# Performance work log

Hardware: AMD Instinct MI355X
Metric: run time of the kernel (lower is better)

The kernel has to match this reference:

```python
import jax, jax.numpy as jnp
import numpy as np

NODE_LEN = 200000; E = 1000000; BATCH = 128; NT = 2048
IN_FEATS = 256; HID = 128; L1 = 13; L2 = 30; NHEAD = 8; GAMMA = 0.1


def _type_att(xs, W, b, q):
    # xs: [N, T, d] -> [N, d]; type-level (semantic) attention
    s = jnp.einsum('ntd,d->nt', jnp.tanh(xs @ W + b), q)
    a = jax.nn.softmax(s, axis=1)
    return jnp.einsum('nt,ntd->nd', a, xs)


def _add_att(qv, kv, Wq, Wk, v):
    # qv: [N, d], kv: [N, L, d] -> [N, d]; additive attention over L
    t = jnp.tanh((qv @ Wq)[:, None, :] + kv @ Wk)
    a = jax.nn.softmax(jnp.einsum('nld,d->nl', t, v), axis=1)
    return jnp.einsum('nl,nld->nd', a, kv)


def _mha(h, W, b):
    # h: [N, L, D]; W: [4, D, D] (q,k,v,o); b: [4, D]
    N, L, D = h.shape
    hd = D // NHEAD
    def proj(i):
        return (h @ W[i] + b[i]).reshape(N, L, NHEAD, hd).transpose(0, 2, 1, 3)
    q, k, v = proj(0), proj(1), proj(2)
    a = jax.nn.softmax(jnp.einsum('nhld,nhmd->nhlm', q, k) / jnp.sqrt(jnp.float32(hd)), axis=-1)
    o = jnp.einsum('nhlm,nhmd->nhld', a, v).transpose(0, 2, 1, 3).reshape(N, L, D)
    return o @ W[3] + b[3]


def _forward(x, edge_index, batch, rootindex, type_x0, type_x1, type_x2, root1, parent1,
             root2, parent2, type_x3, root3, type_x4, root4, adj,
             W1, b1, W2, b2, mha_W, mha_b, att_Wq, att_Wk, att_v, fuse_W, fuse_b,
             gat_W, gat_a_src, gat_a_dst, ta_W, ta_b, ta_q, gc2_W, gc2_b, fin_W, fin_b):
    n = x.shape[0]
    loop = jnp.arange(n, dtype=edge_index.dtype)
    row = jnp.concatenate([edge_index[0], loop])
    col = jnp.concatenate([edge_index[1], loop])
    deg = jax.ops.segment_sum(jnp.ones(row.shape[0], x.dtype), col, num_segments=n)
    dinv = jax.lax.rsqrt(jnp.maximum(deg, 1.0))
    norm = (dinv[row] * dinv[col])[:, None]

    def gcn(h, W, b):
        m = (h @ W)[row] * norm
        return jax.ops.segment_sum(m, col, num_segments=n) + b

    h1 = gcn(x, W1, b1)                          # conv1
    root_extend = h1[rootindex[batch]]           # per-graph root broadcast (replaces python loop)
    h = jax.nn.relu(jnp.concatenate([h1, root_extend], axis=1))
    h2 = jax.nn.relu(gcn(h, W2, b2))             # conv2
    # sentinel zero row == eye(node_len+1, node_len) one-hot gather semantics
    hp = jnp.concatenate([h2, jnp.zeros((1, h2.shape[1]), h2.dtype)], axis=0)

    x0 = [hp[type_x0]]
    for i, (tx, rid, pid) in enumerate([(type_x1, root1, parent1), (type_x2, root2, parent2)]):
        lst, rt, pr = hp[tx], hp[rid], hp[pid]
        ids = jnp.stack([pr, rt], axis=1)        # [N, 2, d]
        att = _add_att(lst, ids, att_Wq[i], att_Wk[i], att_v[i])
        alpha = jax.nn.sigmoid(jnp.concatenate([lst, att], axis=-1) @ fuse_W[i] + fuse_b[i])[:, None]
        x0.append(alpha * lst + (1.0 - alpha) * att)
    for i, (tx, rid) in enumerate([(type_x3, root3), (type_x4, root4)]):
        seq = _mha(hp[tx], mha_W[i], mha_b[i])   # [N, L, d]
        rt = hp[rid]
        att = _add_att(rt, seq, att_Wq[2 + i], att_Wk[2 + i], att_v[2 + i])
        alpha = jax.nn.sigmoid(jnp.concatenate([rt, att], axis=-1) @ fuse_W[2 + i] + fuse_b[2 + i])[:, None]
        x0.append(alpha * rt + (1.0 - alpha) * att)
    x0.append(hp[type_x0])

    # heterogeneous graph attention conv (gc1) + per-type attention fusion (at1)
    H = jnp.stack([x0[t] @ gat_W[t] for t in range(6)])  # [6, NT, d]
    mask = adj > 0
    x1 = []
    for t1 in range(6):
        msgs = []
        for t2 in range(6):
            e = (H[t1] @ gat_a_src[t1, t2])[:, None] + (H[t2] @ gat_a_dst[t1, t2])[None, :]
            s = jnp.where(mask[t1, t2], jax.nn.leaky_relu(e, negative_slope=GAMMA), -1e9)
            msgs.append(jax.nn.softmax(s, axis=1) @ H[t2])
        m = jnp.stack(msgs, axis=1)                      # [NT, 6, d]
        x1.append(jax.nn.relu(_type_att(m, ta_W[t1], ta_b[t1], ta_q[t1])))
    X1 = jnp.stack(x1)                                   # [6, NT, d]

    # second hop: dense GraphConvolution (gc2) + at2; only type 5 feeds the head
    hx = X1 @ gc2_W
    msgs5 = jnp.einsum('snm,smd->snd', adj[5], hx) + gc2_b
    x2_5 = _type_att(msgs5.transpose(1, 0, 2), ta_W[11], ta_b[11], ta_q[11])
    return jax.nn.log_softmax(x2_5 @ fin_W + fin_b, axis=-1)


def setup_inputs() -> dict:
    key = jax.random.key(0)
    ks = jax.random.split(key, 32)
    f32 = jnp.float32
    x = jax.random.normal(ks[0], (NODE_LEN, IN_FEATS), f32)
    edge_index = jax.random.randint(ks[1], (2, E), 0, NODE_LEN, dtype=jnp.int32)
    batch = jax.random.randint(ks[2], (NODE_LEN,), 0, BATCH, dtype=jnp.int32)
    rootindex = jax.random.randint(ks[3], (BATCH,), 0, NODE_LEN, dtype=jnp.int32)
    idx = lambda k, shape: jax.random.randint(k, shape, 0, NODE_LEN, dtype=jnp.int32)
    type_x0 = idx(ks[4], (NT,)); type_x1 = idx(ks[5], (NT,)); type_x2 = idx(ks[6], (NT,))
    root1 = idx(ks[7], (NT,)); parent1 = idx(ks[8], (NT,))
    root2 = idx(ks[9], (NT,)); parent2 = idx(ks[10], (NT,))
    type_x3 = idx(ks[11], (NT, L1)); root3 = idx(ks[12], (NT,))
    type_x4 = idx(ks[13], (NT, L2)); root4 = idx(ks[14], (NT,))
    adj = (jax.random.uniform(ks[15], (6, 6, NT, NT)) < 0.02).astype(f32)
    p = lambda k, shape: 0.02 * jax.random.normal(k, shape, f32)
    W1 = p(ks[16], (IN_FEATS, HID)); b1 = jnp.zeros((HID,), f32)
    W2 = p(ks[17], (2 * HID, HID)); b2 = jnp.zeros((HID,), f32)
    mha_W = p(ks[18], (2, 4, HID, HID)); mha_b = jnp.zeros((2, 4, HID), f32)
    att_Wq = p(ks[19], (4, HID, HID)); att_Wk = p(ks[20], (4, HID, HID)); att_v = p(ks[21], (4, HID))
    fuse_W = p(ks[22], (4, 2 * HID)); fuse_b = jnp.zeros((4,), f32)
    gat_W = p(ks[23], (6, HID, HID)); gat_a_src = p(ks[24], (6, 6, HID)); gat_a_dst = p(ks[25], (6, 6, HID))
    ta_W = p(ks[26], (12, HID, HID)); ta_b = jnp.zeros((12, HID), f32); ta_q = p(ks[27], (12, HID))
    gc2_W = p(ks[28], (HID, HID)); gc2_b = jnp.zeros((HID,), f32)
    fin_W = p(ks[29], (HID, 4)); fin_b = jnp.zeros((4,), f32)
    return dict(x=x, edge_index=edge_index, batch=batch, rootindex=rootindex,
                type_x0=type_x0, type_x1=type_x1, type_x2=type_x2,
                root1=root1, parent1=parent1, root2=root2, parent2=parent2,
                type_x3=type_x3, root3=root3, type_x4=type_x4, root4=root4, adj=adj,
                W1=W1, b1=b1, W2=W2, b2=b2, mha_W=mha_W, mha_b=mha_b,
                att_Wq=att_Wq, att_Wk=att_Wk, att_v=att_v, fuse_W=fuse_W, fuse_b=fuse_b,
                gat_W=gat_W, gat_a_src=gat_a_src, gat_a_dst=gat_a_dst,
                ta_W=ta_W, ta_b=ta_b, ta_q=ta_q, gc2_W=gc2_W, gc2_b=gc2_b,
                fin_W=fin_W, fin_b=fin_b)


def reference(x, edge_index, batch, rootindex, type_x0, type_x1, type_x2, root1, parent1,
              root2, parent2, type_x3, root3, type_x4, root4, adj,
              W1, b1, W2, b2, mha_W, mha_b, att_Wq, att_Wk, att_v, fuse_W, fuse_b,
              gat_W, gat_a_src, gat_a_dst, ta_W, ta_b, ta_q, gc2_W, gc2_b, fin_W, fin_b):
    return _forward(x, edge_index, batch, rootindex, type_x0, type_x1, type_x2, root1, parent1,
                    root2, parent2, type_x3, root3, type_x4, root4, adj,
                    W1, b1, W2, b2, mha_W, mha_b, att_Wq, att_Wk, att_v, fuse_W, fuse_b,
                    gat_W, gat_a_src, gat_a_dst, ta_W, ta_b, ta_q, gc2_W, gc2_b, fin_W, fin_b)
```

## Files before the change

### kernel.cpp

```cpp
#include <hip/hip_runtime.h>
#include <hip/hip_bf16.h>
#include <math.h>


typedef unsigned short u16;
typedef unsigned int   u32;
typedef __attribute__((ext_vector_type(8))) short short8;
typedef __attribute__((ext_vector_type(4))) float f32x4;

#define NNODE 200000
#define NEDGE 1000000
#define NTT   2048

static constexpr size_t MiB = 1024ull * 1024ull;

enum : unsigned {
    O_W1 = 0,         O_b1 = 32768,     O_W2 = 32896,     O_b2 = 65664,
    O_mhaW = 65792,   O_mhab = 196864,  O_attWq = 197888, O_attWk = 263424,
    O_attv = 328960,  O_fuseW = 329472, O_fuseb = 330496, O_gatW = 330504,
    O_asrc = 428808,  O_adst = 433416,  O_taW = 438024,   O_tab = 634632,
    O_taq = 636168,   O_gc2W = 637704,  O_gc2b = 654088,  O_finW = 654216,
    O_finb = 654728
};
enum : unsigned {
    T_W1 = 0,          T_W2 = 32768,     T_mhaW = 65536,   T_attWk = 196608,
    T_gatW = 262144,   T_taW = 360448,   T_gc2W = 557056
};

__device__ __forceinline__ float b2f(u16 u) { return __uint_as_float(((u32)u) << 16); }
__device__ __forceinline__ u16 f2b(float f) {
    u32 u = __float_as_uint(f);
    u32 r = (u + 0x7fffu + ((u >> 16) & 1u)) >> 16;
    return (u16)r;
}

__device__ __forceinline__ float wsum(float v) {
#pragma unroll
    for (int m = 1; m < 64; m <<= 1) v += __shfl_xor(v, m, 64);
    return v;
}
__device__ __forceinline__ float bsum128(float v, float* s) {
    v = wsum(v);
    __syncthreads();
    if ((threadIdx.x & 63) == 0) s[threadIdx.x >> 6] = v;
    __syncthreads();
    return s[0] + s[1];
}
__device__ __forceinline__ float bmax128(float v, float* s) {
#pragma unroll
    for (int m = 1; m < 64; m <<= 1) v = fmaxf(v, __shfl_xor(v, m, 64));
    __syncthreads();
    if ((threadIdx.x & 63) == 0) s[threadIdx.x >> 6] = v;
    __syncthreads();
    return fmaxf(s[0], s[1]);
}

__global__ __launch_bounds__(256) void probe_k(const void* xsrc, int* flag) {
    __shared__ int cnt;
    if (threadIdx.x == 0) cnt = 0;
    __syncthreads();
    int c = 0;
    for (int i = threadIdx.x; i < 4096; i += 256) {
        float v = fabsf(b2f(((const u16*)xsrc)[2 * i]));
        if (v > 1e-6f && v < 100.f) c++;
    }
    atomicAdd(&cnt, c);
    __syncthreads();
    if (threadIdx.x == 0) {
        flag[0] = (cnt < 2048) ? 1 : 0;
        flag[1] = 1;
    }
}

struct CEnt { const void* src; unsigned dstOff; unsigned cnt; };
struct CTab { CEnt e[21]; };
struct TEnt { const void* src; unsigned dstOff; unsigned cnt; int msh; int ksh; };
struct TTab { TEnt e[7]; };
__global__ __launch_bounds__(256) void convp_k(CTab tb, TTab tt, u16* pb, u16* pbT,
                                               const int* flag) {
    bool f32 = flag[0] != 0;
    int stride = gridDim.x * blockDim.x;
    int tid = blockIdx.x * blockDim.x + threadIdx.x;
    for (int k = 0; k < 21; k++) {
        const void* s = tb.e[k].src;
        unsigned off = tb.e[k].dstOff, n = tb.e[k].cnt;
        for (unsigned i = tid; i < n; i += stride)
            pb[off + i] = f32 ? f2b(((const float*)s)[i]) : ((const u16*)s)[i];
    }
    for (int k = 0; k < 7; k++) {
        const void* s = tt.e[k].src;
        unsigned off = tt.e[k].dstOff, n = tt.e[k].cnt;
        int msh = tt.e[k].msh, ksh = tt.e[k].ksh;
        for (unsigned i = tid; i < n; i += stride) {
            unsigned mat = i >> msh, r = i & ((1u << msh) - 1);
            unsigned kk = r >> 7, nn = r & 127;
            unsigned dst = (mat << msh) + (nn << ksh) + kk;
            pbT[off + dst] = f32 ? f2b(((const float*)s)[i]) : ((const u16*)s)[i];
        }
    }
}

template <int K, bool OBF>
__global__ __launch_bounds__(256) void gemm_bf16(const void* __restrict__ A,
                                                 const u16* __restrict__ WT,
                                                 const u16* __restrict__ bias,
                                                 void* __restrict__ Cv, int M,
                                                 const int* flagp) {
    constexpr int LW = 40;
    __shared__ u16 Al[128 * LW];
    __shared__ u16 Bl[128 * LW];
    const int tid = threadIdx.x;
    const int lane = tid & 63, wv = tid >> 6;
    const int row0 = blockIdx.x * 128;
    const int m16 = lane & 15, oct = lane >> 4;
    const bool aF32 = flagp && (flagp[0] != 0);

    f32x4 acc[2][8];
#pragma unroll
    for (int s = 0; s < 2; s++)
#pragma unroll
        for (int t = 0; t < 8; t++) acc[s][t] = (f32x4){0.f, 0.f, 0.f, 0.f};

    const int r = tid >> 1, kk16 = (tid & 1) * 16;
    const int gr = row0 + r;
    const bool rowOk = (gr < M);

    for (int k0 = 0; k0 < K; k0 += 32) {
        {
            uint4 d0 = {0, 0, 0, 0}, d1 = {0, 0, 0, 0};
            if (rowOk) {
                if (aF32) {
                    const float4* s4 = (const float4*)((const float*)A + (size_t)gr * K + k0 + kk16);
                    union { uint4 v[2]; u16 u[16]; } t;
#pragma unroll
                    for (int q = 0; q < 4; q++) {
                        float4 f = s4[q];
                        t.u[q * 4 + 0] = f2b(f.x); t.u[q * 4 + 1] = f2b(f.y);
                        t.u[q * 4 + 2] = f2b(f.z); t.u[q * 4 + 3] = f2b(f.w);
                    }
                    d0 = t.v[0];
                    d1 = t.v[1];
                } else {
                    const uint4* src = (const uint4*)((const u16*)A + (size_t)gr * K + k0 + kk16);
                    d0 = src[0];
                    d1 = src[1];
                }
            }
            *(uint4*)&Al[r * LW + kk16] = d0;
            *(uint4*)&Al[r * LW + kk16 + 8] = d1;
        }
        {
            const uint4* wsrc = (const uint4*)(WT + (size_t)r * K + k0 + kk16);
            *(uint4*)&Bl[r * LW + kk16] = wsrc[0];
            *(uint4*)&Bl[r * LW + kk16 + 8] = wsrc[1];
        }
        __syncthreads();

        short8 af0 = *(const short8*)&Al[(wv * 32 + m16) * LW + oct * 8];
        short8 af1 = *(const short8*)&Al[(wv * 32 + 16 + m16) * LW + oct * 8];
        short8 bf[8];
#pragma unroll
        for (int t = 0; t < 8; t++)
            bf[t] = *(const short8*)&Bl[(t * 16 + m16) * LW + oct * 8];
#pragma unroll
        for (int t = 0; t < 8; t++) {
            acc[0][t] = __builtin_amdgcn_mfma_f32_16x16x32_bf16(af0, bf[t], acc[0][t], 0, 0, 0);
            acc[1][t] = __builtin_amdgcn_mfma_f32_16x16x32_bf16(af1, bf[t], acc[1][t], 0, 0, 0);
        }
        __syncthreads();
    }

    float bv[8];
#pragma unroll
    for (int t = 0; t < 8; t++) bv[t] = bias ? b2f(bias[t * 16 + m16]) : 0.f;
#pragma unroll
    for (int s = 0; s < 2; s++)
#pragma unroll
        for (int t = 0; t < 8; t++)
#pragma unroll
            for (int rr = 0; rr < 4; rr++) {
                int orow = row0 + wv * 32 + s * 16 + oct * 4 + rr;
                if (orow < M) {
                    float val = acc[s][t][rr] + bv[t];
                    size_t idx = (size_t)orow * 128 + t * 16 + m16;
                    if (OBF) ((u16*)Cv)[idx] = f2b(val);
                    else     ((float*)Cv)[idx] = val;
                }
            }
}

template <int K, bool OBF>
__global__ __launch_bounds__(256) void gemm_bat_k(const u16* __restrict__ A0, size_t Astride,
                                                  const u16* __restrict__ W0, unsigned Wstride,
                                                  const u16* __restrict__ bias0, unsigned bStride,
                                                  void* __restrict__ Cv, size_t Cstride,
                                                  int M) {
    constexpr int LW = 40;
    __shared__ u16 Al[128 * LW];
    __shared__ u16 Bl[128 * LW];
    const int y = blockIdx.y;
    const u16* A = A0 + (size_t)y * Astride;
    const u16* WT = W0 + (size_t)y * Wstride;
    const u16* bias = bias0 ? (bias0 + (size_t)y * bStride) : nullptr;
    const size_t cbase = (size_t)y * Cstride;
    const int tid = threadIdx.x;
    const int lane = tid & 63, wv = tid >> 6;
    const int row0 = blockIdx.x * 128;
    const int m16 = lane & 15, oct = lane >> 4;

    f32x4 acc[2][8];
#pragma unroll
    for (int s = 0; s < 2; s++)
#pragma unroll
        for (int t = 0; t < 8; t++) acc[s][t] = (f32x4){0.f, 0.f, 0.f, 0.f};

    const int r = tid >> 1, kk16 = (tid & 1) * 16;
    const int gr = row0 + r;
    const bool rowOk = (gr < M);

    for (int k0 = 0; k0 < K; k0 += 32) {
        {
            uint4 d0 = {0, 0, 0, 0}, d1 = {0, 0, 0, 0};
            if (rowOk) {
                const uint4* src = (const uint4*)(A + (size_t)gr * K + k0 + kk16);
                d0 = src[0];
                d1 = src[1];
            }
            *(uint4*)&Al[r * LW + kk16] = d0;
            *(uint4*)&Al[r * LW + kk16 + 8] = d1;
        }
        {
            const uint4* wsrc = (const uint4*)(WT + (size_t)r * K + k0 + kk16);
            *(uint4*)&Bl[r * LW + kk16] = wsrc[0];
            *(uint4*)&Bl[r * LW + kk16 + 8] = wsrc[1];
        }
        __syncthreads();

        short8 af0 = *(const short8*)&Al[(wv * 32 + m16) * LW + oct * 8];
        short8 af1 = *(const short8*)&Al[(wv * 32 + 16 + m16) * LW + oct * 8];
        short8 bf[8];
#pragma unroll
        for (int t = 0; t < 8; t++)
            bf[t] = *(const short8*)&Bl[(t * 16 + m16) * LW + oct * 8];
#pragma unroll
        for (int t = 0; t < 8; t++) {
            acc[0][t] = __builtin_amdgcn_mfma_f32_16x16x32_bf16(af0, bf[t], acc[0][t], 0, 0, 0);
            acc[1][t] = __builtin_amdgcn_mfma_f32_16x16x32_bf16(af1, bf[t], acc[1][t], 0, 0, 0);
        }
        __syncthreads();
    }

    float bv[8];
#pragma unroll
    for (int t = 0; t < 8; t++) bv[t] = bias ? b2f(bias[t * 16 + m16]) : 0.f;
#pragma unroll
    for (int s = 0; s < 2; s++)
#pragma unroll
        for (int t = 0; t < 8; t++)
#pragma unroll
            for (int rr = 0; rr < 4; rr++) {
                int orow = row0 + wv * 32 + s * 16 + oct * 4 + rr;
                if (orow < M) {
                    float val = acc[s][t][rr] + bv[t];
                    size_t idx = cbase + (size_t)orow * 128 + t * 16 + m16;
                    if (OBF) ((u16*)Cv)[idx] = f2b(val);
                    else     ((float*)Cv)[idx] = val;
                }
            }
}

__global__ __launch_bounds__(256) void gemm_conv2(const u16* __restrict__ h1r,
                                                  const int* __restrict__ batch,
                                                  const int* __restrict__ rootindex,
                                                  const u16* __restrict__ WT,
                                                  u16* __restrict__ C, int M) {
    constexpr int LW = 40;
    __shared__ u16 Al[128 * LW];
    __shared__ u16 Bl[128 * LW];
    const int tid = threadIdx.x;
    const int lane = tid & 63, wv = tid >> 6;
    const int row0 = blockIdx.x * 128;
    const int m16 = lane & 15, oct = lane >> 4;

    f32x4 acc[2][8];
#pragma unroll
    for (int s = 0; s < 2; s++)
#pragma unroll
        for (int t = 0; t < 8; t++) acc[s][t] = (f32x4){0.f, 0.f, 0.f, 0.f};

    const int r = tid >> 1, kk16 = (tid & 1) * 16;
    const int gr = row0 + r;
    const u16* pSelf = nullptr; const u16* pRoot = nullptr;
    if (gr < M) {
        pSelf = h1r + (size_t)gr * 128;
        pRoot = h1r + (size_t)rootindex[batch[gr]] * 128;
    }

    for (int k0 = 0; k0 < 256; k0 += 32) {
        {
            int kg = k0 + kk16;
            uint4 d0 = {0, 0, 0, 0}, d1 = {0, 0, 0, 0};
            if (pSelf) {
                const u16* sp = (kg < 128) ? (pSelf + kg) : (pRoot + kg - 128);
                d0 = ((const uint4*)sp)[0];
                d1 = ((const uint4*)sp)[1];
            }
            *(uint4*)&Al[r * LW + kk16] = d0;
            *(uint4*)&Al[r * LW + kk16 + 8] = d1;
        }
        {
            const uint4* wsrc = (const uint4*)(WT + (size_t)r * 256 + k0 + kk16);
            *(uint4*)&Bl[r * LW + kk16] = wsrc[0];
            *(uint4*)&Bl[r * LW + kk16 + 8] = wsrc[1];
        }
        __syncthreads();

        short8 af0 = *(const short8*)&Al[(wv * 32 + m16) * LW + oct * 8];
        short8 af1 = *(const short8*)&Al[(wv * 32 + 16 + m16) * LW + oct * 8];
        short8 bf[8];
#pragma unroll
        for (int t = 0; t < 8; t++)
            bf[t] = *(const short8*)&Bl[(t * 16 + m16) * LW + oct * 8];
#pragma unroll
        for (int t = 0; t < 8; t++) {
            acc[0][t] = __builtin_amdgcn_mfma_f32_16x16x32_bf16(af0, bf[t], acc[0][t], 0, 0, 0);
            acc[1][t] = __builtin_amdgcn_mfma_f32_16x16x32_bf16(af1, bf[t], acc[1][t], 0, 0, 0);
        }
        __syncthreads();
    }
#pragma unroll
    for (int s = 0; s < 2; s++)
#pragma unroll
        for (int t = 0; t < 8; t++)
#pragma unroll
            for (int rr = 0; rr < 4; rr++) {
                int orow = row0 + wv * 32 + s * 16 + oct * 4 + rr;
                if (orow < M)
                    C[(size_t)orow * 128 + t * 16 + m16] = f2b(acc[s][t][rr]);
            }
}

__global__ __launch_bounds__(256) void hist_k(const int* __restrict__ ei,
                                              int* __restrict__ cnt) {
    int e = blockIdx.x * 256 + threadIdx.x;
    if (e < NEDGE) atomicAdd(&cnt[ei[NEDGE + e]], 1);
}
__global__ __launch_bounds__(256) void scan1_k(const int* __restrict__ cnt,
                                               int* __restrict__ bsum) {
    int t = threadIdx.x;
    int base = blockIdx.x * 1024 + t * 4;
    int s = 0;
#pragma unroll
    for (int q = 0; q < 4; q++) {
        int i = base + q;
        if (i < NNODE) s += cnt[i];
    }
#pragma unroll
    for (int m = 1; m < 64; m <<= 1) s += __shfl_xor(s, m, 64);
    __shared__ int ws_[4];
    if ((t & 63) == 0) ws_[t >> 6] = s;
    __syncthreads();
    if (t == 0) bsum[blockIdx.x] = ws_[0] + ws_[1] + ws_[2] + ws_[3];
}
__global__ __launch_bounds__(64) void scan2_k(const int* __restrict__ bsum,
                                              int* __restrict__ bofs, int nb,
                                              int* __restrict__ rowptrN) {
    if (threadIdx.x == 0) {
        int r = 0;
        for (int i = 0; i < nb; i++) { int v = bsum[i]; bofs[i] = r; r += v; }
        *rowptrN = r;
    }
}
__global__ __launch_bounds__(256) void scan3_k(const int* __restrict__ cnt,
                                               const int* __restrict__ bofs,
                                               int* __restrict__ rowptr,
                                               int* __restrict__ cursor,
                                               float* __restrict__ dinv) {
    int t = threadIdx.x, lane = t & 63, wv = t >> 6;
    int base = blockIdx.x * 1024 + t * 4;
    int v[4];
    int s = 0;
#pragma unroll
    for (int q = 0; q < 4; q++) {
        int i = base + q;
        v[q] = (i < NNODE) ? cnt[i] : 0;
        s += v[q];
    }
    int inc = s;
#pragma unroll
    for (int d = 1; d < 64; d <<= 1) {
        int u = __shfl_up(inc, d, 64);
        if (lane >= d) inc += u;
    }
    __shared__ int wsum_[4];
    if (lane == 63) wsum_[wv] = inc;
    __syncthreads();
    int wofs = 0;
    for (int w = 0; w < wv; w++) wofs += wsum_[w];
    int ex = bofs[blockIdx.x] + wofs + inc - s;
#pragma unroll
    for (int q = 0; q < 4; q++) {
        int i = base + q;
        if (i < NNODE) {
            rowptr[i] = ex;
            cursor[i] = ex;
            dinv[i] = rsqrtf((float)(v[q] + 1));
        }
        ex += v[q];
    }
}
__global__ __launch_bounds__(256) void fill_k(const int* __restrict__ ei,
                                              int* __restrict__ cursor,
                                              int* __restrict__ csr_src) {
    int e = blockIdx.x * 256 + threadIdx.x;
    if (e < NEDGE) {
        int col = ei[NEDGE + e];
        int pos = atomicAdd(&cursor[col], 1);
        csr_src[pos] = ei[e];
    }
}
template <bool OBF>
__global__ __launch_bounds__(256) void gather_gcn_k(const u16* __restrict__ xwb,
                                                    const int* __restrict__ rowptr,
                                                    const int* __restrict__ csr_src,
                                                    const float* __restrict__ dinv,
                                                    const u16* __restrict__ bias,
                                                    void* __restrict__ out) {
    int node = blockIdx.x * 4 + (threadIdx.x >> 6);
    if (node >= NNODE) return;
    int lane = threadIdx.x & 63;
    int beg = rowptr[node], end = rowptr[node + 1];
    int cnt = end - beg;
    if (cnt < 0) cnt = 0;
    if (cnt > 2048) cnt = 2048;
    end = beg + cnt;
    float di = dinv[node];
    u32 pk = *(const u32*)&xwb[(size_t)node * 128 + lane * 2];
    float selfn = di * di;
    float a0 = b2f((u16)(pk & 0xffffu)) * selfn;
    float a1 = b2f((u16)(pk >> 16)) * selfn;
    int myrow = 0; float mynrm = 0.f;
    if (lane < cnt) {
        myrow = csr_src[beg + lane];
        mynrm = dinv[myrow] * di;
    }
    int n0 = cnt < 64 ? cnt : 64;
    for (int j = 0; j < n0; j++) {
        int row = __shfl(myrow, j, 64);
        float nrm = __shfl(mynrm, j, 64);
        u32 p2 = *(const u32*)&xwb[(size_t)row * 128 + lane * 2];
        a0 += b2f((u16)(p2 & 0xffffu)) * nrm;
        a1 += b2f((u16)(p2 >> 16)) * nrm;
    }
    for (int j = beg + 64; j < end; j++) {
        int row = csr_src[j];
        float nrm = dinv[row] * di;
        u32 p2 = *(const u32*)&xwb[(size_t)row * 128 + lane * 2];
        a0 += b2f((u16)(p2 & 0xffffu)) * nrm;
        a1 += b2f((u16)(p2 >> 16)) * nrm;
    }
    a0 = fmaxf(a0 + b2f(bias[lane * 2]), 0.f);
    a1 = fmaxf(a1 + b2f(bias[lane * 2 + 1]), 0.f);
    if (OBF) {
        u32 w = (u32)f2b(a0) | ((u32)f2b(a1) << 16);
        *(u32*)&((u16*)out)[(size_t)node * 128 + lane * 2] = w;
    } else {
        float* op = (float*)out + (size_t)node * 128 + lane * 2;
        op[0] = a0;
        op[1] = a1;
    }
}

__global__ __launch_bounds__(256) void x0copy_k(const float* h2, const int* tx, u16* x0) {
    int idx = blockIdx.x * 256 + threadIdx.x;
    int n = idx >> 7, c = idx & 127;
    u16 v = f2b(h2[(size_t)tx[n] * 128 + c]);
    x0[idx] = v;
    x0[5 * NTT * 128 + idx] = v;
}
__global__ __launch_bounds__(256) void gather_seq_k(const float* h2, const int* tx,
                                                    u16* seqb, int total) {
    int idx = blockIdx.x * 256 + threadIdx.x;
    if (idx >= total) return;
    int node = tx[idx >> 7];
    seqb[idx] = f2b(h2[(size_t)node * 128 + (idx & 127)]);
}
__global__ __launch_bounds__(128) void addatt12_k(const float* __restrict__ h2,
                                                  const int* tx, const int* rid, const int* pid,
                                                  const u16* __restrict__ Wq,
                                                  const u16* __restrict__ Wk,
                                                  const u16* __restrict__ vv,
                                                  const u16* __restrict__ fw,
                                                  const u16* fbp, int fbi,
                                                  u16* __restrict__ out) {
    int n = blockIdx.x, c = threadIdx.x;
    __shared__ float ls[128], pr[128], rt[128], red[2];
    ls[c] = h2[(size_t)tx[n] * 128 + c];
    pr[c] = h2[(size_t)pid[n] * 128 + c];
    rt[c] = h2[(size_t)rid[n] * 128 + c];
    __syncthreads();
    float qc = 0.f;
    for (int k = 0; k < 128; k++) qc += ls[k] * b2f(Wq[k * 128 + c]);
    float vc = b2f(vv[c]);
    float u0 = qc, u1 = qc;
    for (int k = 0; k < 128; k++) {
        float wk = b2f(Wk[k * 128 + c]);
        u0 += pr[k] * wk;
        u1 += rt[k] * wk;
    }
    float s0 = bsum128(tanhf(u0) * vc, red);
    float s1 = bsum128(tanhf(u1) * vc, red);
    float mx = fmaxf(s0, s1);
    float e0 = expf(s0 - mx), e1 = expf(s1 - mx);
    float iz = 1.f / (e0 + e1);
    float att = (e0 * pr[c] + e1 * rt[c]) * iz;
    float pa = ls[c] * b2f(fw[c]) + att * b2f(fw[128 + c]);
    float alpha = 1.f / (1.f + expf(-(bsum128(pa, red) + b2f(fbp[fbi]))));
    out[(size_t)n * 128 + c] = f2b(alpha * ls[c] + (1.f - alpha) * att);
}
__global__ __launch_bounds__(64) void mha_attn_k(const u16* __restrict__ q,
                                                 const u16* __restrict__ k,
                                                 const u16* __restrict__ v,
                                                 u16* __restrict__ ao, int L) {
    int n = blockIdx.x, h = blockIdx.y, t = threadIdx.x;
    __shared__ float qs[30][16], ks[30][16], vs[30][16], sc[30][30];
    for (int e = t; e < L * 16; e += 64) {
        int l = e >> 4, d = e & 15;
        size_t base = ((size_t)n * L + l) * 128 + h * 16 + d;
        qs[l][d] = b2f(q[base]);
        ks[l][d] = b2f(k[base]);
        vs[l][d] = b2f(v[base]);
    }
    __syncthreads();
    for (int e = t; e < L * L; e += 64) {
        int l = e / L, m = e % L;
        float s = 0.f;
#pragma unroll
        for (int d = 0; d < 16; d++) s += qs[l][d] * ks[m][d];
        sc[l][m] = s * 0.25f;
    }
    __syncthreads();
    if (t < L) {
        float mx = -3e38f;
        for (int m = 0; m < L; m++) mx = fmaxf(mx, sc[t][m]);
        float z = 0.f;
        for (int m = 0; m < L; m++) { float w = expf(sc[t][m] - mx); sc[t][m] = w; z += w; }
        float izz = 1.f / z;
        for (int m = 0; m < L; m++) sc[t][m] *= izz;
    }
    __syncthreads();
    for (int e = t; e < L * 16; e += 64) {
        int l = e >> 4, d = e & 15;
        float o = 0.f;
        for (int m = 0; m < L; m++) o += sc[l][m] * vs[m][d];
        ao[((size_t)n * L + l) * 128 + h * 16 + d] = f2b(o);
    }
}
__global__ __launch_bounds__(128) void addatt_root_k(const u16* __restrict__ seqo,
                                                     const u16* __restrict__ kpre,
                                                     const float* __restrict__ h2,
                                                     const int* rid,
                                                     const u16* __restrict__ Wq,
                                                     const u16* __restrict__ vv,
                                                     const u16* __restrict__ fw,
                                                     const u16* fbp, int fbi, int L,
                                                     u16* __restrict__ out) {
    int n = blockIdx.x, c = threadIdx.x;
    __shared__ float rt[128], sl[32], red[2];
    rt[c] = h2[(size_t)rid[n] * 128 + c];
    __syncthreads();
    float qc = 0.f;
    for (int k = 0; k < 128; k++) qc += rt[k] * b2f(Wq[k * 128 + c]);
    float vc = b2f(vv[c]);
    for (int l = 0; l < L; l++) {
        float u = qc + b2f(kpre[((size_t)n * L + l) * 128 + c]);
        float s = bsum128(tanhf(u) * vc, red);
        if (c == 0) sl[l] = s;
    }
    __syncthreads();
    float mx = -3e38f;
    for (int l = 0; l < L; l++) mx = fmaxf(mx, sl[l]);
    float z = 0.f;
    for (int l = 0; l < L; l++) z += expf(sl[l] - mx);
    float att = 0.f;
    for (int l = 0; l < L; l++)
        att += expf(sl[l] - mx) * b2f(seqo[((size_t)n * L + l) * 128 + c]);
    att /= z;
    float pa = rt[c] * b2f(fw[c]) + att * b2f(fw[128 + c]);
    float alpha = 1.f / (1.f + expf(-(bsum128(pa, red) + b2f(fbp[fbi]))));
    out[(size_t)n * 128 + c] = f2b(alpha * rt[c] + (1.f - alpha) * att);
}
__global__ __launch_bounds__(128) void gat_e2_k(const float* __restrict__ H,
                                                const u16* __restrict__ asrc,
                                                const u16* __restrict__ adst,
                                                float* esrc, float* edst) {
    int p = blockIdx.y, t1 = p / 6, t2 = p % 6;
    int t = threadIdx.x;
    __shared__ float vs[128], vd[128];
    vs[t] = b2f(asrc[p * 128 + t]);
    vd[t] = b2f(adst[p * 128 + t]);
    __syncthreads();
    int row = t >> 2, part = t & 3;
    int i = blockIdx.x * 32 + row;
    const float4* r1 = (const float4*)(H + ((size_t)t1 * NTT + i) * 128 + part * 32);
    const float4* r2 = (const float4*)(H + ((size_t)t2 * NTT + i) * 128 + part * 32);
    float s1 = 0.f, s2 = 0.f;
#pragma unroll
    for (int q = 0; q < 8; q++) {
        float4 a = r1[q], b = r2[q];
        int kb = part * 32 + q * 4;
        s1 += a.x * vs[kb] + a.y * vs[kb + 1] + a.z * vs[kb + 2] + a.w * vs[kb + 3];
        s2 += b.x * vd[kb] + b.y * vd[kb + 1] + b.z * vd[kb + 2] + b.w * vd[kb + 3];
    }
    s1 += __shfl_xor(s1, 1, 64); s1 += __shfl_xor(s1, 2, 64);
    s2 += __shfl_xor(s2, 1, 64); s2 += __shfl_xor(s2, 2, 64);
    if (part == 0) {
        esrc[p * NTT + i] = s1;
        edst[p * NTT + i] = s2;
    }
}
__global__ __launch_bounds__(128) void gc1_attn_k(const void* __restrict__ adjv,
                                                  const float* __restrict__ H,
                                                  const float* __restrict__ esrc,
                                                  const float* __restrict__ edst,
                                                  u16* __restrict__ msgs,
                                                  const int* flagp) {
    int i = blockIdx.x, p = blockIdx.y, t = threadIdx.x;
    int t2 = p % 6;
    const bool f32 = flagp[0] != 0;
    size_t rowoff = ((size_t)p * NTT + i) * NTT;
    const float* edp = edst + p * NTT;
    float es = esrc[p * NTT + i];
    __shared__ int nzj[2048];
    __shared__ float nzs[2048];
    __shared__ int cnt;
    __shared__ float red[2];
    if (t == 0) cnt = 0;
    __syncthreads();
    int j0 = t * 16;
    float av[16];
    if (f32) {
        const float4* af = (const float4*)((const float*)adjv + rowoff + j0);
#pragma unroll
        for (int q = 0; q < 4; q++) {
            float4 d = af[q];
            av[q * 4 + 0] = d.x; av[q * 4 + 1] = d.y;
            av[q * 4 + 2] = d.z; av[q * 4 + 3] = d.w;
        }
    } else {
        const u16* ab = (const u16*)adjv + rowoff + j0;
        union { uint4 v; u16 u[8]; } a0, a1;
        a0.v = *(const uint4*)(ab);
        a1.v = *(const uint4*)(ab + 8);
#pragma unroll
        for (int q = 0; q < 16; q++) av[q] = b2f(q < 8 ? a0.u[q] : a1.u[q - 8]);
    }
    float lmax = -3e38f;
#pragma unroll
    for (int jj = 0; jj < 16; jj++) {
        if (av[jj] > 0.f) {
            int j = j0 + jj;
            float e = es + edp[j];
            float sv = e > 0.f ? e : 0.1f * e;
            lmax = fmaxf(lmax, sv);
            int kk = atomicAdd(&cnt, 1);
            nzj[kk] = j;
            nzs[kk] = sv;
        }
    }
    float mx = bmax128(lmax, red);
    int nnz = cnt;
    float psum = 0.f;
    for (int k = t; k < nnz; k += 128) {
        float w = expf(nzs[k] - mx);
        nzs[k] = w;
        psum += w;
    }
    float Z = bsum128(psum, red);
    const float* Ht = H + (size_t)t2 * NTT * 128;
    float acc = 0.f;
    if (nnz > 0) {
        for (int k = 0; k < nnz; k++) acc += nzs[k] * Ht[(size_t)nzj[k] * 128 + t];
        acc /= Z;
    } else {
        for (int j = 0; j < NTT; j++) acc += Ht[(size_t)j * 128 + t];
        acc *= (1.f / 2048.f);
    }
    msgs[((size_t)p * NTT + i) * 128 + t] = f2b(acc);
}
__global__ __launch_bounds__(128) void at1_lite_k(const u16* __restrict__ msgs,
                                                  const u16* __restrict__ ubuf,
                                                  const u16* __restrict__ taq,
                                                  u16* __restrict__ X1) {
    int n = blockIdx.x, t1 = blockIdx.y, c = threadIdx.x;
    __shared__ float sv[6], red[2];
    float qcv = b2f(taq[t1 * 128 + c]);
    for (int t2 = 0; t2 < 6; t2++) {
        float u = b2f(ubuf[(((size_t)t1 * 6 + t2) * NTT + n) * 128 + c]);
        float s = bsum128(tanhf(u) * qcv, red);
        if (c == 0) sv[t2] = s;
    }
    __syncthreads();
    float mx = -3e38f;
    for (int t2 = 0; t2 < 6; t2++) mx = fmaxf(mx, sv[t2]);
    float z = 0.f;
    for (int t2 = 0; t2 < 6; t2++) z += expf(sv[t2] - mx);
    float o = 0.f;
    for (int t2 = 0; t2 < 6; t2++)
        o += expf(sv[t2] - mx) * b2f(msgs[(((size_t)t1 * 6 + t2) * NTT + n) * 128 + c]);
    o /= z;
    X1[((size_t)t1 * NTT + n) * 128 + c] = f2b(fmaxf(o, 0.f));
}
__global__ __launch_bounds__(128) void gc2_agg_k(const void* __restrict__ adjv,
                                                 size_t adjBase,
                                                 const float* __restrict__ hx,
                                                 const u16* __restrict__ bias,
                                                 float* __restrict__ msgs5,
                                                 const int* flagp) {
    int i = blockIdx.x, s = blockIdx.y, t = threadIdx.x;
    const bool f32 = flagp[0] != 0;
    size_t rowoff = adjBase + ((size_t)s * NTT + i) * NTT;
    __shared__ int nzj[2048];
    __shared__ float nzw[2048];
    __shared__ int cnt;
    if (t == 0) cnt = 0;
    __syncthreads();
    int j0 = t * 16;
    float av[16];
    if (f32) {
        const float4* af = (const float4*)((const float*)adjv + rowoff + j0);
#pragma unroll
        for (int q = 0; q < 4; q++) {
            float4 d = af[q];
            av[q * 4 + 0] = d.x; av[q * 4 + 1] = d.y;
            av[q * 4 + 2] = d.z; av[q * 4 + 3] = d.w;
        }
    } else {
        const u16* ab = (const u16*)adjv + rowoff + j0;
        union { uint4 v; u16 u[8]; } a0, a1;
        a0.v = *(const uint4*)(ab);
        a1.v = *(const uint4*)(ab + 8);
#pragma unroll
        for (int q = 0; q < 16; q++) av[q] = b2f(q < 8 ? a0.u[q] : a1.u[q - 8]);
    }
#pragma unroll
    for (int jj = 0; jj < 16; jj++) {
        if (av[jj] != 0.f) {
            int kk = atomicAdd(&cnt, 1);
            nzj[kk] = j0 + jj;
            nzw[kk] = av[jj];
        }
    }
    __syncthreads();
    const float* hxs = hx + (size_t)s * NTT * 128;
    float acc = 0.f;
    int nnz = cnt;
    for (int k = 0; k < nnz; k++) acc += nzw[k] * hxs[(size_t)nzj[k] * 128 + t];
    msgs5[((size_t)s * NTT + i) * 128 + t] = acc + b2f(bias[t]);
}
__global__ __launch_bounds__(128) void at2_head_lite_k(const float* __restrict__ msgs5,
                                                       const u16* __restrict__ ubuf2,
                                                       const u16* __restrict__ taq,
                                                       const u16* __restrict__ finW,
                                                       const u16* __restrict__ finb,
                                                       float* __restrict__ out) {
    int n = blockIdx.x, c = threadIdx.x;
    __shared__ float sv[6], red[2];
    float qcv = b2f(taq[11 * 128 + c]);
    for (int s = 0; s < 6; s++) {
        float u = b2f(ubuf2[((size_t)s * NTT + n) * 128 + c]);
        float sc = bsum128(tanhf(u) * qcv, red);
        if (c == 0) sv[s] = sc;
    }
    __syncthreads();
    float mx = -3e38f;
    for (int s = 0; s < 6; s++) mx = fmaxf(mx, sv[s]);
    float z = 0.f;
    for (int s = 0; s < 6; s++) z += expf(sv[s] - mx);
    float x2c = 0.f;
    for (int s = 0; s < 6; s++)
        x2c += expf(sv[s] - mx) * msgs5[((size_t)s * NTT + n) * 128 + c];
    x2c /= z;
    float l0 = bsum128(x2c * b2f(finW[c * 4 + 0]), red) + b2f(finb[0]);
    float l1 = bsum128(x2c * b2f(finW[c * 4 + 1]), red) + b2f(finb[1]);
    float l2 = bsum128(x2c * b2f(finW[c * 4 + 2]), red) + b2f(finb[2]);
    float l3 = bsum128(x2c * b2f(finW[c * 4 + 3]), red) + b2f(finb[3]);
    float m4 = fmaxf(fmaxf(l0, l1), fmaxf(l2, l3));
    float ls = logf(expf(l0 - m4) + expf(l1 - m4) + expf(l2 - m4) + expf(l3 - m4)) + m4;
    if (c < 4) {
        float v = (c == 0) ? l0 : (c == 1) ? l1 : (c == 2) ? l2 : l3;
        out[n * 4 + c] = v - ls;
    }
}

extern "C" void kernel_launch(void* const* d_in, const int* in_sizes, int n_in,
                              void* d_out, int out_size, void* d_ws, size_t ws_size,
                              hipStream_t stream) {
    const void* x       = d_in[0];
    const int* ei       = (const int*)d_in[1];
    const int* batch    = (const int*)d_in[2];
    const int* rootidx  = (const int*)d_in[3];
    const int* type_x0  = (const int*)d_in[4];
    const int* type_x1  = (const int*)d_in[5];
    const int* type_x2  = (const int*)d_in[6];
    const int* root1    = (const int*)d_in[7];
    const int* parent1  = (const int*)d_in[8];
    const int* root2    = (const int*)d_in[9];
    const int* parent2  = (const int*)d_in[10];
    const int* type_x3  = (const int*)d_in[11];
    const int* root3    = (const int*)d_in[12];
    const int* type_x4  = (const int*)d_in[13];
    const int* root4    = (const int*)d_in[14];
    const void* adj     = d_in[15];

    char* ws = (char*)d_ws;
    int*   flag = (int*)(ws);
    u16*   pb   = (u16*)  (ws + 64 * 1024);
    float* dinv = (float*)(ws + 2 * MiB);
    u16*   xwb  = (u16*)  (ws + 3 * MiB);
    float* h2   = (float*)(ws + 52 * MiB);
    u16*   h1r  = (u16*)  (ws + 52 * MiB);
    int*   cnt_i   = (int*)(ws + 150 * MiB);
    int*   rowptr  = (int*)(ws + 151 * MiB);
    int*   cursor  = (int*)(ws + 152 * MiB);
    int*   csr_src = (int*)(ws + 153 * MiB);
    int*   bsum    = (int*)(ws + 158 * MiB);
    int*   bofs    = (int*)(ws + 158 * MiB + 4096);
    u16*   seqb = (u16*)  (ws + 3 * MiB);
    u16*   qb   = (u16*)  (ws + 18 * MiB);
    u16*   kb   = (u16*)  (ws + 33 * MiB);
    u16*   vb   = (u16*)  (ws + 150 * MiB);
    u16*   aob  = (u16*)  (ws + 165 * MiB);
    u16*   seqo = (u16*)  (ws + 18 * MiB);
    u16*   kpre = (u16*)  (ws + 33 * MiB);
    u16*   x0b  = (u16*)  (ws + 180 * MiB);
    u16*   X1b  = (u16*)  (ws + 183 * MiB);
    float* Hb   = (float*)(ws + 52 * MiB);
    float* esrc = (float*)(ws + 58 * MiB);
    float* edst = (float*)(ws + 59 * MiB);
    u16*   msgs = (u16*)  (ws + 60 * MiB);
    u16*   ubuf = (u16*)  (ws + 78 * MiB);
    float* hx   = (float*)(ws + 96 * MiB);
    float* msg5 = (float*)(ws + 102 * MiB);
    u16*   ubuf2= (u16*)  (ws + 60 * MiB);
    u16*   pbT  = (u16*)  (ws + 186 * MiB);

    probe_k<<<1, 256, 0, stream>>>(x, flag);
    CTab tb;
    int kk = 0;
    auto add = [&](int i, unsigned off, unsigned n) {
        tb.e[kk].src = d_in[i]; tb.e[kk].dstOff = off; tb.e[kk].cnt = n; kk++;
    };
    add(16, O_W1, 32768);   add(17, O_b1, 128);     add(18, O_W2, 32768);
    add(19, O_b2, 128);     add(20, O_mhaW, 131072);add(21, O_mhab, 1024);
    add(22, O_attWq, 65536);add(23, O_attWk, 65536);add(24, O_attv, 512);
    add(25, O_fuseW, 1024); add(26, O_fuseb, 4);    add(27, O_gatW, 98304);
    add(28, O_asrc, 4608);  add(29, O_adst, 4608);  add(30, O_taW, 196608);
    add(31, O_tab, 1536);   add(32, O_taq, 1536);   add(33, O_gc2W, 16384);
    add(34, O_gc2b, 128);   add(35, O_finW, 512);   add(36, O_finb, 4);
    TTab tt;
    int tk = 0;
    auto addt = [&](int i, unsigned off, unsigned n, int msh, int ksh) {
        tt.e[tk].src = d_in[i]; tt.e[tk].dstOff = off; tt.e[tk].cnt = n;
        tt.e[tk].msh = msh; tt.e[tk].ksh = ksh; tk++;
    };
    addt(16, T_W1, 32768, 15, 8);
    addt(18, T_W2, 32768, 15, 8);
    addt(20, T_mhaW, 131072, 14, 7);
    addt(23, T_attWk, 65536, 14, 7);
    addt(27, T_gatW, 98304, 14, 7);
    addt(30, T_taW, 196608, 14, 7);
    addt(33, T_gc2W, 16384, 14, 7);
    convp_k<<<256, 256, 0, stream>>>(tb, tt, pb, pbT, flag);

    const int NB = (NNODE + 1023) / 1024;
    hipMemsetAsync(cnt_i, 0, (size_t)NNODE * 4, stream);
    hist_k<<<(NEDGE + 255) / 256, 256, 0, stream>>>(ei, cnt_i);
    scan1_k<<<NB, 256, 0, stream>>>(cnt_i, bsum);
    scan2_k<<<1, 64, 0, stream>>>(bsum, bofs, NB, rowptr + NNODE);
    scan3_k<<<NB, 256, 0, stream>>>(cnt_i, bofs, rowptr, cursor, dinv);
    fill_k<<<(NEDGE + 255) / 256, 256, 0, stream>>>(ei, cursor, csr_src);

    gemm_bf16<256, true><<<(NNODE + 127) / 128, 256, 0, stream>>>(x, pbT + T_W1, (const u16*)nullptr, xwb, NNODE, flag);
    gather_gcn_k<true><<<(NNODE + 3) / 4, 256, 0, stream>>>(xwb, rowptr, csr_src, dinv, pb + O_b1, h1r);

    gemm_conv2<<<(NNODE + 127) / 128, 256, 0, stream>>>(h1r, batch, rootidx, pbT + T_W2, xwb, NNODE);
    gather_gcn_k<false><<<(NNODE + 3) / 4, 256, 0, stream>>>(xwb, rowptr, csr_src, dinv, pb + O_b2, h2);

    x0copy_k<<<(NTT * 128) / 256, 256, 0, stream>>>(h2, type_x0, x0b);
    addatt12_k<<<NTT, 128, 0, stream>>>(h2, type_x1, root1, parent1,
                                        pb + O_attWq, pb + O_attWk, pb + O_attv,
                                        pb + O_fuseW, pb + O_fuseb, 0,
                                        x0b + 1 * NTT * 128);
    addatt12_k<<<NTT, 128, 0, stream>>>(h2, type_x2, root2, parent2,
                                        pb + O_attWq + 16384, pb + O_attWk + 16384,
                                        pb + O_attv + 128, pb + O_fuseW + 256,
                                        pb + O_fuseb, 1,
                                        x0b + 2 * NTT * 128);
    for (int i = 0; i < 2; i++) {
        int L = i ? 30 : 13;
        const int* tx = i ? type_x4 : type_x3;
        const int* rt = i ? root4 : root3;
        int M = NTT * L;
        gather_seq_k<<<(M * 128 + 255) / 256, 256, 0, stream>>>(h2, tx, seqb, M * 128);
        gemm_bf16<128, true><<<(M + 127) / 128, 256, 0, stream>>>(seqb, pbT + T_mhaW + (i * 4 + 0) * 16384,
                                                                  pb + O_mhab + (i * 4 + 0) * 128, qb, M, nullptr);
        gemm_bf16<128, true><<<(M + 127) / 128, 256, 0, stream>>>(seqb, pbT + T_mhaW + (i * 4 + 1) * 16384,
                                                                  pb + O_mhab + (i * 4 + 1) * 128, kb, M, nullptr);
        gemm_bf16<128, true><<<(M + 127) / 128, 256, 0, stream>>>(seqb, pbT + T_mhaW + (i * 4 + 2) * 16384,
                                                                  pb + O_mhab + (i * 4 + 2) * 128, vb, M, nullptr);
        mha_attn_k<<<dim3(NTT, 8), 64, 0, stream>>>(qb, kb, vb, aob, L);
        gemm_bf16<128, true><<<(M + 127) / 128, 256, 0, stream>>>(aob, pbT + T_mhaW + (i * 4 + 3) * 16384,
                                                                  pb + O_mhab + (i * 4 + 3) * 128, seqo, M, nullptr);
        gemm_bf16<128, true><<<(M + 127) / 128, 256, 0, stream>>>(seqo, pbT + T_attWk + (2 + i) * 16384,
                                                                  (const u16*)nullptr, kpre, M, nullptr);
        addatt_root_k<<<NTT, 128, 0, stream>>>(seqo, kpre, h2, rt,
                                               pb + O_attWq + (2 + i) * 16384,
                                               pb + O_attv + (2 + i) * 128,
                                               pb + O_fuseW + (2 + i) * 256,
                                               pb + O_fuseb, 2 + i, L,
                                               x0b + (3 + i) * NTT * 128);
    }

    gemm_bat_k<128, false><<<dim3(NTT / 128, 6), 256, 0, stream>>>(
        x0b, (size_t)NTT * 128, pbT + T_gatW, 16384, (const u16*)nullptr, 0,
        Hb, (size_t)NTT * 128, NTT);
    gat_e2_k<<<dim3(NTT / 32, 36), 128, 0, stream>>>(Hb, pb + O_asrc, pb + O_adst, esrc, edst);
    gc1_attn_k<<<dim3(NTT, 36), 128, 0, stream>>>(adj, Hb, esrc, edst, msgs, flag);
    gemm_bat_k<128, true><<<dim3((6 * NTT) / 128, 6), 256, 0, stream>>>(
        msgs, (size_t)6 * NTT * 128, pbT + T_taW, 16384, pb + O_tab, 128,
        ubuf, (size_t)6 * NTT * 128, 6 * NTT);
    at1_lite_k<<<dim3(NTT, 6), 128, 0, stream>>>(msgs, ubuf, pb + O_taq, X1b);
    gemm_bf16<128, false><<<(6 * NTT) / 128, 256, 0, stream>>>(X1b, pbT + T_gc2W, (const u16*)nullptr, hx, 6 * NTT, nullptr);
    gc2_agg_k<<<dim3(NTT, 6), 128, 0, stream>>>(adj, (size_t)5 * 6 * NTT * NTT, hx,
                                                pb + O_gc2b, msg5, flag);
    gemm_bf16<128, true><<<(6 * NTT) / 128, 256, 0, stream>>>(msg5, pbT + T_taW + 11 * 16384,
                                                              pb + O_tab + 11 * 128, ubuf2, 6 * NTT, flag + 1);
    at2_head_lite_k<<<NTT, 128, 0, stream>>>(msg5, ubuf2, pb + O_taq,
                                             pb + O_finW, pb + O_finb, (float*)d_out);
}
```

Before: 2.001 ms.

## Cache sparse adjacency lists in gc1 for gc2, batch QKV and addatt launches

While scanning the adjacency block for the last relation group, gc1_attn_k now records nonzero column indices and weights (capped per row) into a workspace. gc2_agg_k then reuses these compact lists instead of rereading the dense adjacency rows from memory. The change also merges the three Q/K/V projection GEMMs into one multi-slab launch, merges the two addatt12 launches via blockIdx.y, and unrolls the gather loops by four. In exchange it adds shared-memory atomics and global writes in gc1, and it depends on rows having at most 256 nonzeros to use the fast path.

Measured after the change: 2.007 ms. Within noise of the previous version (+0.3%).

```diff
diff --git a/kernel.cpp b/kernel.cpp
--- a/kernel.cpp
+++ b/kernel.cpp
@@ -11,6 +11,7 @@
 #define NNODE 200000
 #define NEDGE 1000000
 #define NTT   2048
+#define G2CAP 256
 
 static constexpr size_t MiB = 1024ull * 1024ull;
 
@@ -266,6 +267,77 @@
                     if (OBF) ((u16*)Cv)[idx] = f2b(val);
                     else     ((float*)Cv)[idx] = val;
                 }
+            }
+}
+
+struct GSlab { const u16* A; const u16* WT; const u16* bias; u16* C; int M; };
+struct GDesc { GSlab s[3]; };
+template <int K>
+__global__ __launch_bounds__(256) void gemm_ms_k(GDesc d) {
+    constexpr int LW = 40;
+    __shared__ u16 Al[128 * LW];
+    __shared__ u16 Bl[128 * LW];
+    const GSlab sl = d.s[blockIdx.y];
+    const int row0 = blockIdx.x * 128;
+    if (row0 >= sl.M) return;
+    const int tid = threadIdx.x;
+    const int lane = tid & 63, wv = tid >> 6;
+    const int m16 = lane & 15, oct = lane >> 4;
+
+    f32x4 acc[2][8];
+#pragma unroll
+    for (int s = 0; s < 2; s++)
+#pragma unroll
+        for (int t = 0; t < 8; t++) acc[s][t] = (f32x4){0.f, 0.f, 0.f, 0.f};
+
+    const int r = tid >> 1, kk16 = (tid & 1) * 16;
+    const int gr = row0 + r;
+    const bool rowOk = (gr < sl.M);
+
+    for (int k0 = 0; k0 < K; k0 += 32) {
+        {
+            uint4 d0 = {0, 0, 0, 0}, d1 = {0, 0, 0, 0};
+            if (rowOk) {
+                const uint4* src = (const uint4*)(sl.A + (size_t)gr * K + k0 + kk16);
+                d0 = src[0];
+                d1 = src[1];
+            }
+            *(uint4*)&Al[r * LW + kk16] = d0;
+            *(uint4*)&Al[r * LW + kk16 + 8] = d1;
+        }
+        {
+            const uint4* wsrc = (const uint4*)(sl.WT + (size_t)r * K + k0 + kk16);
+            *(uint4*)&Bl[r * LW + kk16] = wsrc[0];
+            *(uint4*)&Bl[r * LW + kk16 + 8] = wsrc[1];
+        }
+        __syncthreads();
+
+        short8 af0 = *(const short8*)&Al[(wv * 32 + m16) * LW + oct * 8];
+        short8 af1 = *(const short8*)&Al[(wv * 32 + 16 + m16) * LW + oct * 8];
+        short8 bf[8];
+#pragma unroll
+        for (int t = 0; t < 8; t++)
+            bf[t] = *(const short8*)&Bl[(t * 16 + m16) * LW + oct * 8];
+#pragma unroll
+        for (int t = 0; t < 8; t++) {
+            acc[0][t] = __builtin_amdgcn_mfma_f32_16x16x32_bf16(af0, bf[t], acc[0][t], 0, 0, 0);
+            acc[1][t] = __builtin_amdgcn_mfma_f32_16x16x32_bf16(af1, bf[t], acc[1][t], 0, 0, 0);
+        }
+        __syncthreads();
+    }
+
+    float bv[8];
+#pragma unroll
+    for (int t = 0; t < 8; t++) bv[t] = sl.bias ? b2f(sl.bias[t * 16 + m16]) : 0.f;
+#pragma unroll
+    for (int s = 0; s < 2; s++)
+#pragma unroll
+        for (int t = 0; t < 8; t++)
+#pragma unroll
+            for (int rr = 0; rr < 4; rr++) {
+                int orow = row0 + wv * 32 + s * 16 + oct * 4 + rr;
+                if (orow < sl.M)
+                    sl.C[(size_t)orow * 128 + t * 16 + m16] = f2b(acc[s][t][rr] + bv[t]);
             }
 }
 
@@ -486,14 +558,20 @@
     seqb[idx] = f2b(h2[(size_t)node * 128 + (idx & 127)]);
 }
 __global__ __launch_bounds__(128) void addatt12_k(const float* __restrict__ h2,
-                                                  const int* tx, const int* rid, const int* pid,
-                                                  const u16* __restrict__ Wq,
-                                                  const u16* __restrict__ Wk,
-                                                  const u16* __restrict__ vv,
-                                                  const u16* __restrict__ fw,
-                                                  const u16* fbp, int fbi,
-                                                  u16* __restrict__ out) {
-    int n = blockIdx.x, c = threadIdx.x;
+                                                  const int* tx0, const int* rid0, const int* pid0,
+                                                  const int* tx1, const int* rid1, const int* pid1,
+                                                  const u16* __restrict__ pbp,
+                                                  u16* __restrict__ x0b) {
+    int n = blockIdx.x, c = threadIdx.x, y = blockIdx.y;
+    const int* tx = y ? tx1 : tx0;
+    const int* rid = y ? rid1 : rid0;
+    const int* pid = y ? pid1 : pid0;
+    const u16* Wq = pbp + O_attWq + y * 16384;
+    const u16* Wk = pbp + O_attWk + y * 16384;
+    const u16* vv = pbp + O_attv + y * 128;
+    const u16* fw = pbp + O_fuseW + y * 256;
+    const u16* fbp = pbp + O_fuseb;
+    u16* out = x0b + (size_t)(1 + y) * NTT * 128;
     __shared__ float ls[128], pr[128], rt[128], red[2];
     ls[c] = h2[(size_t)tx[n] * 128 + c];
     pr[c] = h2[(size_t)pid[n] * 128 + c];
@@ -515,7 +593,7 @@
     float iz = 1.f / (e0 + e1);
     float att = (e0 * pr[c] + e1 * rt[c]) * iz;
     float pa = ls[c] * b2f(fw[c]) + att * b2f(fw[128 + c]);
-    float alpha = 1.f / (1.f + expf(-(bsum128(pa, red) + b2f(fbp[fbi]))));
+    float alpha = 1.f / (1.f + expf(-(bsum128(pa, red) + b2f(fbp[y]))));
     out[(size_t)n * 128 + c] = f2b(alpha * ls[c] + (1.f - alpha) * att);
 }
 __global__ __launch_bounds__(64) void mha_attn_k(const u16* __restrict__ q,
@@ -624,6 +702,9 @@
                                                   const float* __restrict__ esrc,
                                                   const float* __restrict__ edst,
                                                   u16* __restrict__ msgs,
+                                                  int* __restrict__ g2cnt,
+                                                  int* __restrict__ g2j,
+                                                  float* __restrict__ g2w,
                                                   const int* flagp) {
     int i = blockIdx.x, p = blockIdx.y, t = threadIdx.x;
     int t2 = p % 6;
@@ -633,9 +714,9 @@
     float es = esrc[p * NTT + i];
     __shared__ int nzj[2048];
     __shared__ float nzs[2048];
-    __shared__ int cnt;
+    __shared__ int cnt, cnt2;
     __shared__ float red[2];
-    if (t == 0) cnt = 0;
+    if (t == 0) { cnt = 0; cnt2 = 0; }
     __syncthreads();
     int j0 = t * 16;
     float av[16];
@@ -655,6 +736,8 @@
 #pragma unroll
         for (int q = 0; q < 16; q++) av[q] = b2f(q < 8 ? a0.u[q] : a1.u[q - 8]);
     }
+    const bool spill = (p >= 30);
+    size_t g2base = spill ? ((size_t)(p - 30) * NTT + i) * G2CAP : 0;
     float lmax = -3e38f;
 #pragma unroll
     for (int jj = 0; jj < 16; jj++) {
@@ -667,9 +750,17 @@
             nzj[kk] = j;
             nzs[kk] = sv;
         }
+        if (spill && av[jj] != 0.f) {
+            int q = atomicAdd(&cnt2, 1);
+            if (q < G2CAP) {
+                g2j[g2base + q] = j0 + jj;
+                g2w[g2base + q] = av[jj];
+            }
+        }
     }
     float mx = bmax128(lmax, red);
     int nnz = cnt;
+    if (spill && t == 0) g2cnt[(p - 30) * NTT + i] = cnt2;
     float psum = 0.f;
     for (int k = t; k < nnz; k += 128) {
         float w = expf(nzs[k] - mx);
@@ -680,7 +771,17 @@
     const float* Ht = H + (size_t)t2 * NTT * 128;
     float acc = 0.f;
     if (nnz > 0) {
-        for (int k = 0; k < nnz; k++) acc += nzs[k] * Ht[(size_t)nzj[k] * 128 + t];
+        int k = 0;
+        for (; k + 4 <= nnz; k += 4) {
+            int ja = nzj[k], jb = nzj[k + 1], jc = nzj[k + 2], jd = nzj[k + 3];
+            float wa = nzs[k], wb = nzs[k + 1], wc = nzs[k + 2], wd = nzs[k + 3];
+            float ha = Ht[(size_t)ja * 128 + t];
+            float hb = Ht[(size_t)jb * 128 + t];
+            float hc = Ht[(size_t)jc * 128 + t];
+            float hd = Ht[(size_t)jd * 128 + t];
+            acc += wa * ha + wb * hb + wc * hc + wd * hd;
+        }
+        for (; k < nnz; k++) acc += nzs[k] * Ht[(size_t)nzj[k] * 128 + t];
         acc /= Z;
     } else {
         for (int j = 0; j < NTT; j++) acc += Ht[(size_t)j * 128 + t];
@@ -715,14 +816,38 @@
                                                  size_t adjBase,
                                                  const float* __restrict__ hx,
                                                  const u16* __restrict__ bias,
+                                                 const int* __restrict__ g2cnt,
+                                                 const int* __restrict__ g2j,
+                                                 const float* __restrict__ g2w,
                                                  float* __restrict__ msgs5,
                                                  const int* flagp) {
     int i = blockIdx.x, s = blockIdx.y, t = threadIdx.x;
-    const bool f32 = flagp[0] != 0;
-    size_t rowoff = adjBase + ((size_t)s * NTT + i) * NTT;
     __shared__ int nzj[2048];
     __shared__ float nzw[2048];
     __shared__ int cnt;
+    int pre = g2cnt[s * NTT + i];
+    const float* hxs = hx + (size_t)s * NTT * 128;
+    if (pre <= G2CAP) {
+        size_t g2base = ((size_t)s * NTT + i) * G2CAP;
+        for (int k = t; k < pre; k += 128) {
+            nzj[k] = g2j[g2base + k];
+            nzw[k] = g2w[g2base + k];
+        }
+        __syncthreads();
+        float acc = 0.f;
+        int k = 0;
+        for (; k + 4 <= pre; k += 4) {
+            int ja = nzj[k], jb = nzj[k + 1], jc = nzj[k + 2], jd = nzj[k + 3];
+            float wa = nzw[k], wb = nzw[k + 1], wc = nzw[k + 2], wd = nzw[k + 3];
+            acc += wa * hxs[(size_t)ja * 128 + t] + wb * hxs[(size_t)jb * 128 + t]
+                 + wc * hxs[(size_t)jc * 128 + t] + wd * hxs[(size_t)jd * 128 + t];
+        }
+        for (; k < pre; k++) acc += nzw[k] * hxs[(size_t)nzj[k] * 128 + t];
+        msgs5[((size_t)s * NTT + i) * 128 + t] = acc + b2f(bias[t]);
+        return;
+    }
+    const bool f32 = flagp[0] != 0;
+    size_t rowoff = adjBase + ((size_t)s * NTT + i) * NTT;
     if (t == 0) cnt = 0;
     __syncthreads();
     int j0 = t * 16;
@@ -752,7 +877,6 @@
         }
     }
     __syncthreads();
-    const float* hxs = hx + (size_t)s * NTT * 128;
     float acc = 0.f;
     int nnz = cnt;
     for (int k = 0; k < nnz; k++) acc += nzw[k] * hxs[(size_t)nzj[k] * 128 + t];
@@ -842,6 +966,9 @@
     u16*   ubuf = (u16*)  (ws + 78 * MiB);
     float* hx   = (float*)(ws + 96 * MiB);
     float* msg5 = (float*)(ws + 102 * MiB);
+    int*   g2cnt= (int*)  (ws + 108 * MiB);
+    int*   g2j  = (int*)  (ws + 109 * MiB);
+    float* g2w  = (float*)(ws + 122 * MiB);
     u16*   ubuf2= (u16*)  (ws + 60 * MiB);
     u16*   pbT  = (u16*)  (ws + 186 * MiB);
 
@@ -888,27 +1015,23 @@
     gather_gcn_k<false><<<(NNODE + 3) / 4, 256, 0, stream>>>(xwb, rowptr, csr_src, dinv, pb + O_b2, h2);
 
     x0copy_k<<<(NTT * 128) / 256, 256, 0, stream>>>(h2, type_x0, x0b);
-    addatt12_k<<<NTT, 128, 0, stream>>>(h2, type_x1, root1, parent1,
-                                        pb + O_attWq, pb + O_attWk, pb + O_attv,
-                                        pb + O_fuseW, pb + O_fuseb, 0,
-                                        x0b + 1 * NTT * 128);
-    addatt12_k<<<NTT, 128, 0, stream>>>(h2, type_x2, root2, parent2,
-                                        pb + O_attWq + 16384, pb + O_attWk + 16384,
-                                        pb + O_attv + 128, pb + O_fuseW + 256,
-                                        pb + O_fuseb, 1,
-                                        x0b + 2 * NTT * 128);
+    addatt12_k<<<dim3(NTT, 2), 128, 0, stream>>>(h2, type_x1, root1, parent1,
+                                                 type_x2, root2, parent2, pb, x0b);
     for (int i = 0; i < 2; i++) {
         int L = i ? 30 : 13;
         const int* tx = i ? type_x4 : type_x3;
         const int* rt = i ? root4 : root3;
         int M = NTT * L;
         gather_seq_k<<<(M * 128 + 255) / 256, 256, 0, stream>>>(h2, tx, seqb, M * 128);
-        gemm_bf16<128, true><<<(M + 127) / 128, 256, 0, stream>>>(seqb, pbT + T_mhaW + (i * 4 + 0) * 16384,
-                                                                  pb + O_mhab + (i * 4 + 0) * 128, qb, M, nullptr);
-        gemm_bf16<128, true><<<(M + 127) / 128, 256, 0, stream>>>(seqb, pbT + T_mhaW + (i * 4 + 1) * 16384,
-                                                                  pb + O_mhab + (i * 4 + 1) * 128, kb, M, nullptr);
-        gemm_bf16<128, true><<<(M + 127) / 128, 256, 0, stream>>>(seqb, pbT + T_mhaW + (i * 4 + 2) * 16384,
-                                                                  pb + O_mhab + (i * 4 + 2) * 128, vb, M, nullptr);
+        GDesc qkv;
+        for (int pjt = 0; pjt < 3; pjt++) {
+            qkv.s[pjt].A = seqb;
+            qkv.s[pjt].WT = pbT + T_mhaW + (i * 4 + pjt) * 16384;
+            qkv.s[pjt].bias = pb + O_mhab + (i * 4 + pjt) * 128;
+            qkv.s[pjt].C = (pjt == 0) ? qb : (pjt == 1) ? kb : vb;
+            qkv.s[pjt].M = M;
+        }
+        gemm_ms_k<128><<<dim3((M + 127) / 128, 3), 256, 0, stream>>>(qkv);
         mha_attn_k<<<dim3(NTT, 8), 64, 0, stream>>>(qb, kb, vb, aob, L);
         gemm_bf16<128, true><<<(M + 127) / 128, 256, 0, stream>>>(aob, pbT + T_mhaW + (i * 4 + 3) * 16384,
                                                                   pb + O_mhab + (i * 4 + 3) * 128, seqo, M, nullptr);
@@ -919,21 +1042,22 @@
                                                pb + O_attv + (2 + i) * 128,
                                                pb + O_fuseW + (2 + i) * 256,
                                                pb + O_fuseb, 2 + i, L,
-                                               x0b + (3 + i) * NTT * 128);
+                                               x0b + (size_t)(3 + i) * NTT * 128);
     }
 
     gemm_bat_k<128, false><<<dim3(NTT / 128, 6), 256, 0, stream>>>(
         x0b, (size_t)NTT * 128, pbT + T_gatW, 16384, (const u16*)nullptr, 0,
         Hb, (size_t)NTT * 128, NTT);
     gat_e2_k<<<dim3(NTT / 32, 36), 128, 0, stream>>>(Hb, pb + O_asrc, pb + O_adst, esrc, edst);
-    gc1_attn_k<<<dim3(NTT, 36), 128, 0, stream>>>(adj, Hb, esrc, edst, msgs, flag);
+    gc1_attn_k<<<dim3(NTT, 36), 128, 0, stream>>>(adj, Hb, esrc, edst, msgs,
+                                                  g2cnt, g2j, g2w, flag);
     gemm_bat_k<128, true><<<dim3((6 * NTT) / 128, 6), 256, 0, stream>>>(
         msgs, (size_t)6 * NTT * 128, pbT + T_taW, 16384, pb + O_tab, 128,
         ubuf, (size_t)6 * NTT * 128, 6 * NTT);
     at1_lite_k<<<dim3(NTT, 6), 128, 0, stream>>>(msgs, ubuf, pb + O_taq, X1b);
     gemm_bf16<128, false><<<(6 * NTT) / 128, 256, 0, stream>>>(X1b, pbT + T_gc2W, (const u16*)nullptr, hx, 6 * NTT, nullptr);
     gc2_agg_k<<<dim3(NTT, 6), 128, 0, stream>>>(adj, (size_t)5 * 6 * NTT * NTT, hx,
-                                                pb + O_gc2b, msg5, flag);
+                                                pb + O_gc2b, g2cnt, g2j, g2w, msg5, flag);
     gemm_bf16<128, true><<<(6 * NTT) / 128, 256, 0, stream>>>(msg5, pbT + T_taW + 11 * 16384,
                                                               pb + O_tab + 11 * 128, ubuf2, 6 * NTT, flag + 1);
     at2_head_lite_k<<<NTT, 128, 0, stream>>>(msg5, ubuf2, pb + O_taq,
```
